# Kernel optimization log

Hardware: AMD Instinct MI355X
Metric: run time of the kernel (lower is better)

The kernel has to match this reference:

```python
import jax, jax.numpy as jnp
import numpy as np
import math

B, N, D, H = 4, 2048, 256, 4
DH = D // H
EPS = 1e-8


def setup_inputs() -> dict:
    key = jax.random.key(0)
    ks = jax.random.split(key, 8)
    x = jax.random.normal(ks[0], (B, N, D), dtype=jnp.float32)
    # RoPE rotation freqs: exp(i * pos * inv_freq), stored as (cos, sin) pairs -> [N, DH//2, 2]
    d2 = DH // 2
    inv_freq = 1.0 / (10000.0 ** (jnp.arange(d2, dtype=jnp.float32) / d2))
    ang = jnp.arange(N, dtype=jnp.float32)[:, None] * inv_freq[None, :]
    freqs = jnp.stack([jnp.cos(ang), jnp.sin(ang)], axis=-1)  # [N, d2, 2]
    s = 0.02
    g = jnp.ones((D,), dtype=jnp.float32)
    w_qkv = jax.random.normal(ks[1], (D, 3 * D), dtype=jnp.float32) * s
    b_qkv = jnp.zeros((3 * D,), dtype=jnp.float32)
    w_out = jax.random.normal(ks[2], (D, D), dtype=jnp.float32) * s
    b_out = jnp.zeros((D,), dtype=jnp.float32)
    w_gate = jax.random.normal(ks[3], (D, D), dtype=jnp.float32) * s
    b_gate = jnp.zeros((D,), dtype=jnp.float32)
    return {"x": x, "freqs": freqs, "g": g, "w_qkv": w_qkv, "b_qkv": b_qkv,
            "w_out": w_out, "b_out": b_out, "w_gate": w_gate, "b_gate": b_gate}


def _zcrmsnorm(x, g):
    x0 = x - jnp.mean(x, axis=-1, keepdims=True)
    rms = jnp.sqrt(jnp.mean(x0 * x0, axis=-1, keepdims=True) + EPS)
    return x0 / rms * g


def _rope(q, freqs):
    # q: [B,H,N,DH]; freqs: [N,DH//2,2] (cos,sin). Complex multiply on adjacent pairs.
    b, h, n, dh = q.shape
    qp = q.reshape(b, h, n, dh // 2, 2)
    cos = freqs[:n, :, 0][None, None]  # [1,1,N,d2]
    sin = freqs[:n, :, 1][None, None]
    q0, q1 = qp[..., 0], qp[..., 1]
    out = jnp.stack([q0 * cos - q1 * sin, q0 * sin + q1 * cos], axis=-1)
    return out.reshape(b, h, n, dh)


def reference(x, freqs, g, w_qkv, b_qkv, w_out, b_out, w_gate, b_gate):
    b, n, d = x.shape
    h = _zcrmsnorm(x, g)
    qkv = (h @ w_qkv + b_qkv).reshape(b, n, 3, H, DH)
    qkv = jnp.transpose(qkv, (2, 0, 3, 1, 4))  # [3,B,H,N,DH]
    q, k, v = qkv[0], qkv[1], qkv[2]
    q = _rope(q, freqs)
    k = _rope(k, freqs)
    scores = jnp.einsum('bhqd,bhkd->bhqk', q, k) / math.sqrt(DH)
    attn = jax.nn.softmax(scores, axis=-1)  # dropout is identity in eval
    y = jnp.einsum('bhqk,bhkd->bhqd', attn, v)
    y = jnp.transpose(y, (0, 2, 1, 3)).reshape(b, n, d)
    y = y @ w_out + b_out
    gate = jax.nn.sigmoid(h @ w_gate + b_gate)
    return x + gate * y
```

## Files before the change

kernel.cpp:

```cpp
#include <hip/hip_runtime.h>

typedef unsigned short u16;
typedef unsigned int u32;
typedef short short8 __attribute__((ext_vector_type(8)));
typedef float f32x4 __attribute__((ext_vector_type(4)));

#define B_ 4
#define N_ 2048
#define D_ 256
#define H_ 4
#define DH_ 64
#define BN_ 8192

__device__ inline float b2f(u16 u) {
    union { u32 i; float f; } v; v.i = ((u32)u) << 16; return v.f;
}
__device__ inline u16 f2b(float f) {
    union { float f; u32 i; } v; v.f = f;
    return (u16)((v.i + 0x8000u) >> 16);
}
__device__ inline u32 pkbf(float a, float b) {
    union { float f; u32 i; } ua, ub; ua.f = a; ub.f = b;
    return __builtin_amdgcn_perm(ub.i + 0x8000u, ua.i + 0x8000u, 0x07060302u);
}
__device__ inline f32x4 mfma16(short8 a, short8 b, f32x4 c) {
    return __builtin_amdgcn_mfma_f32_16x16x32_bf16(a, b, c, 0, 0, 0);
}

__device__ __forceinline__ void gemm_body(
    int bx, int by, int tid,
    const u16* __restrict__ A, const u16* __restrict__ BT,
    const float* __restrict__ bias, void* __restrict__ Cout,
    int Ntot)
{
    const int wave = tid >> 6, lane = tid & 63;
    const int ln15 = lane & 15, quad = lane >> 4;
    const int m0 = bx * 128 + (wave & 1) * 64;
    const int n0 = by * 128 + (wave >> 1) * 64;

    const f32x4 zero = {0.f, 0.f, 0.f, 0.f};
    f32x4 acc[4][4];
    #pragma unroll
    for (int i = 0; i < 4; ++i)
        #pragma unroll
        for (int j = 0; j < 4; ++j) acc[i][j] = zero;

    #pragma unroll
    for (int k0 = 0; k0 < 256; k0 += 32) {
        const int koff = k0 + quad * 8;
        short8 a[4], b[4];
        #pragma unroll
        for (int i = 0; i < 4; ++i)
            a[i] = *(const short8*)(A + (size_t)(m0 + i * 16 + ln15) * 256 + koff);
        #pragma unroll
        for (int j = 0; j < 4; ++j)
            b[j] = *(const short8*)(BT + (size_t)(n0 + j * 16 + ln15) * 256 + koff);
        #pragma unroll
        for (int i = 0; i < 4; ++i)
            #pragma unroll
            for (int j = 0; j < 4; ++j)
                acc[i][j] = mfma16(a[i], b[j], acc[i][j]);
    }

    #pragma unroll
    for (int i = 0; i < 4; ++i) {
        const int r = m0 + i * 16 + quad * 4;
        #pragma unroll
        for (int j = 0; j < 4; ++j) {
            const int c = n0 + j * 16 + ln15;
            const float bv = bias[c];
            #pragma unroll
            for (int rg = 0; rg < 4; ++rg) {
                const size_t idx = (size_t)(r + rg) * Ntot + c;
                ((u16*)Cout)[idx] = f2b(acc[i][j][rg] + bv);
            }
        }
    }
}

__device__ __forceinline__ void gemm_thin_body(
    int bx, int by, int tid,
    const u16* __restrict__ A, const u16* __restrict__ BT,
    const float* __restrict__ bias, void* __restrict__ Cout,
    const float* __restrict__ xin, const u16* __restrict__ gate,
    int mode)
{
    const int wave = tid >> 6, lane = tid & 63;
    const int ln15 = lane & 15, quad = lane >> 4;
    const int m0 = bx * 64 + (wave & 1) * 32;
    const int n0 = by * 64 + (wave >> 1) * 32;

    const f32x4 zero = {0.f, 0.f, 0.f, 0.f};
    f32x4 acc[2][2];
    #pragma unroll
    for (int i = 0; i < 2; ++i)
        #pragma unroll
        for (int j = 0; j < 2; ++j) acc[i][j] = zero;

    #pragma unroll
    for (int k0 = 0; k0 < 256; k0 += 32) {
        const int koff = k0 + quad * 8;
        short8 a[2], b[2];
        #pragma unroll
        for (int i = 0; i < 2; ++i)
            a[i] = *(const short8*)(A + (size_t)(m0 + i * 16 + ln15) * 256 + koff);
        #pragma unroll
        for (int j = 0; j < 2; ++j)
            b[j] = *(const short8*)(BT + (size_t)(n0 + j * 16 + ln15) * 256 + koff);
        #pragma unroll
        for (int i = 0; i < 2; ++i)
            #pragma unroll
            for (int j = 0; j < 2; ++j)
                acc[i][j] = mfma16(a[i], b[j], acc[i][j]);
    }

    #pragma unroll
    for (int i = 0; i < 2; ++i) {
        const int r = m0 + i * 16 + quad * 4;
        #pragma unroll
        for (int j = 0; j < 2; ++j) {
            const int c = n0 + j * 16 + ln15;
            const float bv = bias[c];
            #pragma unroll
            for (int rg = 0; rg < 4; ++rg) {
                const size_t idx = (size_t)(r + rg) * 256 + c;
                float v = acc[i][j][rg] + bv;
                if (mode == 1) {
                    ((u16*)Cout)[idx] = f2b(1.0f / (1.0f + __expf(-v)));
                } else {
                    ((float*)Cout)[idx] = xin[idx] + b2f(gate[idx]) * v;
                }
            }
        }
    }
}

__global__ __launch_bounds__(256) void gemm_ep(
    const u16* __restrict__ A, const u16* __restrict__ BT,
    const float* __restrict__ bias, void* __restrict__ Cout, int Ntot)
{
    gemm_body(blockIdx.x, blockIdx.y, threadIdx.x, A, BT, bias, Cout, Ntot);
}

__global__ __launch_bounds__(256) void gemm_thin(
    const u16* __restrict__ A, const u16* __restrict__ BT,
    const float* __restrict__ bias, void* __restrict__ Cout,
    const float* __restrict__ xin, const u16* __restrict__ gate, int mode)
{
    gemm_thin_body(blockIdx.x, blockIdx.y, threadIdx.x, A, BT, bias, Cout,
                   xin, gate, mode);
}

__global__ __launch_bounds__(256) void norm_transw_k(
    const float* __restrict__ x, const float* __restrict__ g, u16* __restrict__ h,
    const float* __restrict__ wqkv, const float* __restrict__ wout,
    const float* __restrict__ wgate,
    u16* __restrict__ wqkvT, u16* __restrict__ woutT, u16* __restrict__ wgateT)
{
    if (blockIdx.x < 2048) {
        const int wave = threadIdx.x >> 6, lane = threadIdx.x & 63;
        const int t = blockIdx.x * 4 + wave;
        const float4 u = *(const float4*)(x + (size_t)t * D_ + lane * 4);
        float s  = u.x + u.y + u.z + u.w;
        float s2 = u.x * u.x + u.y * u.y + u.z * u.z + u.w * u.w;
        #pragma unroll
        for (int m = 1; m < 64; m <<= 1) {
            s  += __shfl_xor(s, m);
            s2 += __shfl_xor(s2, m);
        }
        float mean = s * (1.0f / D_);
        float var  = s2 * (1.0f / D_) - mean * mean;
        float rinv = rsqrtf(var + 1e-8f);
        const float4 gv = *(const float4*)(g + lane * 4);
        uint2 o;
        o.x = pkbf((u.x - mean) * rinv * gv.x, (u.y - mean) * rinv * gv.y);
        o.y = pkbf((u.z - mean) * rinv * gv.z, (u.w - mean) * rinv * gv.w);
        *(uint2*)(h + (size_t)t * D_ + lane * 4) = o;
    } else {
        int idx = (blockIdx.x - 2048) * 256 + threadIdx.x;
        if (idx < 768 * 256) {
            int nn = idx >> 8, kk = idx & 255;
            wqkvT[idx] = f2b(wqkv[kk * 768 + nn]);
        }
        idx -= 768 * 256;
        if (idx >= 0 && idx < 256 * 256) {
            int nn = idx >> 8, kk = idx & 255;
            woutT[idx]  = f2b(wout[kk * 256 + nn]);
            wgateT[idx] = f2b(wgate[kk * 256 + nn]);
        }
    }
}

#define QSCALE 0.18033688f
__global__ __launch_bounds__(256) void rope_vt_gate_k(
    const u16* __restrict__ qkv, const float* __restrict__ freqs,
    u16* __restrict__ Q, u16* __restrict__ K, u16* __restrict__ VT,
    const u16* __restrict__ h, const u16* __restrict__ wgateT,
    const float* __restrict__ b_gate, u16* __restrict__ gatb)
{
    __shared__ __align__(16) u16 tile[64 * 65];
    const int blk = blockIdx.x;
    if (blk < 1024) {
        const int idx = blk * 256 + threadIdx.x;
        const int t = idx >> 5, rem = idx & 31;
        const int hh = rem >> 3, s8 = rem & 7;
        const int b = t >> 11, n = t & 2047;

        const float4 f0 = *(const float4*)(freqs + (size_t)n * 64 + s8 * 8);
        const float4 f1 = *(const float4*)(freqs + (size_t)n * 64 + s8 * 8 + 4);

        const u16* qp = qkv + (size_t)t * 768 + hh * 64 + s8 * 8;
        const uint4 qv = *(const uint4*)qp;
        const uint4 kv = *(const uint4*)(qp + 256);

        const size_t off = ((size_t)(b * H_ + hh) * N_ + n) * DH_ + s8 * 8;
        uint4 qo, ko;
        {
            float q0 = b2f((u16)(qv.x & 0xffff)), q1 = b2f((u16)(qv.x >> 16));
            float k0 = b2f((u16)(kv.x & 0xffff)), k1 = b2f((u16)(kv.x >> 16));
            qo.x = pkbf((q0 * f0.x - q1 * f0.y) * QSCALE, (q0 * f0.y + q1 * f0.x) * QSCALE);
            ko.x = pkbf(k0 * f0.x - k1 * f0.y, k0 * f0.y + k1 * f0.x);
        }
        {
            float q0 = b2f((u16)(qv.y & 0xffff)), q1 = b2f((u16)(qv.y >> 16));
            float k0 = b2f((u16)(kv.y & 0xffff)), k1 = b2f((u16)(kv.y >> 16));
            qo.y = pkbf((q0 * f0.z - q1 * f0.w) * QSCALE, (q0 * f0.w + q1 * f0.z) * QSCALE);
            ko.y = pkbf(k0 * f0.z - k1 * f0.w, k0 * f0.w + k1 * f0.z);
        }
        {
            float q0 = b2f((u16)(qv.z & 0xffff)), q1 = b2f((u16)(qv.z >> 16));
            float k0 = b2f((u16)(kv.z & 0xffff)), k1 = b2f((u16)(kv.z >> 16));
            qo.z = pkbf((q0 * f1.x - q1 * f1.y) * QSCALE, (q0 * f1.y + q1 * f1.x) * QSCALE);
            ko.z = pkbf(k0 * f1.x - k1 * f1.y, k0 * f1.y + k1 * f1.x);
        }
        {
            float q0 = b2f((u16)(qv.w & 0xffff)), q1 = b2f((u16)(qv.w >> 16));
            float k0 = b2f((u16)(kv.w & 0xffff)), k1 = b2f((u16)(kv.w >> 16));
            qo.w = pkbf((q0 * f1.z - q1 * f1.w) * QSCALE, (q0 * f1.w + q1 * f1.z) * QSCALE);
            ko.w = pkbf(k0 * f1.z - k1 * f1.w, k0 * f1.w + k1 * f1.z);
        }
        *(uint4*)(Q + off) = qo;
        *(uint4*)(K + off) = ko;
    } else if (blk < 1536) {
        const int id2 = blk - 1024;
        const int bh = id2 & 15;
        const int n0 = (id2 >> 4) * 64;
        const int b = bh >> 2, hh = bh & 3;
        #pragma unroll
        for (int rep = 0; rep < 16; ++rep) {
            int idx = rep * 256 + threadIdx.x;
            int nl = idx >> 6, dh = idx & 63;
            tile[dh * 65 + nl] = qkv[(size_t)(b * N_ + n0 + nl) * 768 + 512 + hh * 64 + dh];
        }
        __syncthreads();
        #pragma unroll
        for (int rep = 0; rep < 16; ++rep) {
            int idx = rep * 256 + threadIdx.x;
            int dh = idx >> 6, nl = idx & 63;
            VT[((size_t)bh * 64 + dh) * N_ + n0 + nl] = tile[dh * 65 + nl];
        }
    } else {
        const int id3 = blk - 1536;
        gemm_thin_body(id3 & 127, id3 >> 7, threadIdx.x, h, wgateT, b_gate,
                       (void*)gatb, (const float*)nullptr, (const u16*)nullptr, 1);
    }
}

__global__ __launch_bounds__(512, 4) void attn_k(
    const u16* __restrict__ Q, const u16* __restrict__ K,
    const u16* __restrict__ VT, float* __restrict__ Op,
    float* __restrict__ lvp)
{
    __shared__ __align__(16) u16 Ks[2][64][64];
    __shared__ __align__(16) u16 Vs[2][64][64];
    __shared__ __align__(16) u16 Pb[8][16 * 88];
    const int tid = threadIdx.x;
    const int wave = tid >> 6, lane = tid & 63;
    const int ln15 = lane & 15, quad = lane >> 4;
    const int id = blockIdx.x;
    const int bh   = ((id & 7) << 1) | ((id >> 3) & 1);
    const int half = (id >> 4) & 1;
    const int q0   = (id >> 5) * 128 + wave * 16;
    const int kt0  = half * 1024;

    const u16* Qh = Q + (size_t)bh * N_ * DH_;
    const u16* Kh = K + (size_t)bh * N_ * DH_;
    const u16* Vh = VT + (size_t)bh * DH_ * N_;

    const short8 bq0 = *(const short8*)(Qh + (size_t)(q0 + ln15) * DH_ + quad * 8);
    const short8 bq1 = *(const short8*)(Qh + (size_t)(q0 + ln15) * DH_ + 32 + quad * 8);

    const f32x4 zero = {0.f, 0.f, 0.f, 0.f};
    f32x4 o[4];
    #pragma unroll
    for (int j = 0; j < 4; ++j) o[j] = zero;
    float lv = 0.f;
    u16* Pw = Pb[wave];

    const int srow = tid >> 3, sq8 = tid & 7;
    const int wc = (sq8 * 8) ^ ((srow & 7) << 3);
    const int swl = (ln15 & 7) << 3;
    const int rc0 = (quad * 8) ^ swl;
    const int rc1 = (quad * 8 + 32) ^ swl;

    {
        uint4 k0 = *(const uint4*)(Kh + (size_t)(kt0 + srow) * DH_ + sq8 * 8);
        uint4 v0 = *(const uint4*)(Vh + (size_t)srow * N_ + kt0 + sq8 * 8);
        *(uint4*)&Ks[0][srow][wc] = k0;
        *(uint4*)&Vs[0][srow][wc] = v0;
    }
    __syncthreads();

    int p = 0;
    for (int c = 0; c < 16; ++c) {
        const int ktn = kt0 + (c + 1) * 64;
        uint4 k0, v0;
        const bool more = (c + 1 < 16);
        if (more) {
            k0 = *(const uint4*)(Kh + (size_t)(ktn + srow) * DH_ + sq8 * 8);
            v0 = *(const uint4*)(Vh + (size_t)srow * N_ + ktn + sq8 * 8);
        }

        f32x4 st[4];
        #pragma unroll
        for (int c4 = 0; c4 < 4; ++c4) {
            short8 ka0 = *(const short8*)&Ks[p][c4 * 16 + ln15][rc0];
            short8 ka1 = *(const short8*)&Ks[p][c4 * 16 + ln15][rc1];
            st[c4] = mfma16(ka0, bq0, zero);
            st[c4] = mfma16(ka1, bq1, st[c4]);
        }
        f32x4 pr[4];
        float rs = 0.f;
        #pragma unroll
        for (int c4 = 0; c4 < 4; ++c4) {
            #pragma unroll
            for (int r = 0; r < 4; ++r) {
                pr[c4][r] = exp2f(st[c4][r]);
                rs += pr[c4][r];
            }
        }
        lv += rs;
        #pragma unroll
        for (int c4 = 0; c4 < 4; ++c4) {
            uint2 w;
            w.x = pkbf(pr[c4][0], pr[c4][1]);
            w.y = pkbf(pr[c4][2], pr[c4][3]);
            *(uint2*)(Pw + ln15 * 88 + c4 * 16 + quad * 4) = w;
        }
        asm volatile("s_waitcnt lgkmcnt(0)" ::: "memory");
        const short8 bp0 = *(const short8*)(Pw + ln15 * 88 + quad * 8);
        const short8 bp1 = *(const short8*)(Pw + ln15 * 88 + 32 + quad * 8);
        #pragma unroll
        for (int j = 0; j < 4; ++j) {
            short8 va0 = *(const short8*)&Vs[p][j * 16 + ln15][rc0];
            short8 va1 = *(const short8*)&Vs[p][j * 16 + ln15][rc1];
            o[j] = mfma16(va0, bp0, o[j]);
            o[j] = mfma16(va1, bp1, o[j]);
        }

        if (more) {
            *(uint4*)&Ks[p ^ 1][srow][wc] = k0;
            *(uint4*)&Vs[p ^ 1][srow][wc] = v0;
        }
        __syncthreads();
        p ^= 1;
    }

    lv += __shfl_xor(lv, 16);
    lv += __shfl_xor(lv, 32);
    const size_t rowo = ((size_t)(half * 16 + bh) * N_ + q0 + ln15) * DH_;
    #pragma unroll
    for (int j = 0; j < 4; ++j) {
        float4 w4 = {o[j][0], o[j][1], o[j][2], o[j][3]};
        *(float4*)(Op + rowo + j * 16 + quad * 4) = w4;
    }
    if (quad == 0) lvp[(size_t)(half * 16 + bh) * N_ + q0 + ln15] = lv;
}

__global__ __launch_bounds__(256) void combine_k(
    const float* __restrict__ Op, const float* __restrict__ lvp,
    u16* __restrict__ yt)
{
    const int t = blockIdx.x * 256 + threadIdx.x;
    const int dh0 = (t & 7) * 8;
    const int q   = (t >> 3) & 2047;
    const int bh  = t >> 14;
    const size_t o0 = ((size_t)bh * N_ + q) * DH_ + dh0;
    const size_t o1 = o0 + (size_t)16 * N_ * DH_;
    const float4 a0 = *(const float4*)(Op + o0);
    const float4 a1 = *(const float4*)(Op + o0 + 4);
    const float4 c0 = *(const float4*)(Op + o1);
    const float4 c1 = *(const float4*)(Op + o1 + 4);
    const float rl = 1.0f / (lvp[(size_t)bh * N_ + q] + lvp[(size_t)(16 + bh) * N_ + q]);
    uint4 w;
    w.x = pkbf((a0.x + c0.x) * rl, (a0.y + c0.y) * rl);
    w.y = pkbf((a0.z + c0.z) * rl, (a0.w + c0.w) * rl);
    w.z = pkbf((a1.x + c1.x) * rl, (a1.y + c1.y) * rl);
    w.w = pkbf((a1.z + c1.z) * rl, (a1.w + c1.w) * rl);
    const int b = bh >> 2, h = bh & 3;
    *(uint4*)(yt + ((size_t)b * N_ + q) * D_ + h * 64 + dh0) = w;
}

extern "C" void kernel_launch(void* const* d_in, const int* in_sizes, int n_in,
                              void* d_out, int out_size, void* d_ws, size_t ws_size,
                              hipStream_t stream) {
    const float* x      = (const float*)d_in[0];
    const float* freqs  = (const float*)d_in[1];
    const float* g      = (const float*)d_in[2];
    const float* w_qkv  = (const float*)d_in[3];
    const float* b_qkv  = (const float*)d_in[4];
    const float* w_out  = (const float*)d_in[5];
    const float* b_out  = (const float*)d_in[6];
    const float* w_gate = (const float*)d_in[7];
    const float* b_gate = (const float*)d_in[8];
    float* out = (float*)d_out;

    char* ws = (char*)d_ws;
    size_t off = 0;
    auto carve = [&](size_t nelem) -> u16* {
        u16* p = (u16*)(ws + off);
        off += ((nelem * 2 + 255) / 256) * 256;
        return p;
    };
    u16* h      = carve((size_t)BN_ * D_);
    u16* qkv    = carve((size_t)BN_ * 768);
    u16* Qb     = carve((size_t)BN_ * D_);
    u16* Kb     = carve((size_t)BN_ * D_);
    u16* VT     = carve((size_t)BN_ * D_);
    u16* gatb   = carve((size_t)BN_ * D_);
    u16* wqkvT  = carve((size_t)768 * 256);
    u16* woutT  = carve((size_t)256 * 256);
    u16* wgateT = carve((size_t)256 * 256);
    float* Op  = (float*)ws;
    float* lvp = (float*)wqkvT;
    u16*   yt  = Qb;

    hipLaunchKernelGGL(norm_transw_k, dim3(3072), dim3(256), 0, stream,
                       x, g, h, w_qkv, w_out, w_gate, wqkvT, woutT, wgateT);
    hipLaunchKernelGGL(gemm_ep, dim3(BN_ / 128, 6), dim3(256), 0, stream,
                       h, wqkvT, b_qkv, (void*)qkv, 768);
    hipLaunchKernelGGL(rope_vt_gate_k, dim3(2048), dim3(256), 0, stream,
                       qkv, freqs, Qb, Kb, VT, h, wgateT, b_gate, gatb);
    hipLaunchKernelGGL(attn_k, dim3(512), dim3(512), 0, stream,
                       Qb, Kb, VT, Op, lvp);
    hipLaunchKernelGGL(combine_k, dim3(1024), dim3(256), 0, stream,
                       Op, lvp, yt);
    hipLaunchKernelGGL(gemm_thin, dim3(128, 4), dim3(256), 0, stream,
                       yt, woutT, b_out, (void*)out, x, gatb, 2);
}
```

Measured before the change: 165.9 us.

## Switch attention to 32x32x16 MFMA with in-register P via permlane32 swap

Rewrites the attention inner loop to use 32x32x16 bf16 MFMA tiles, so each wave handles 32 query rows and the block shrinks to 4 waves. The softmax probabilities are packed to bf16 and rearranged in registers with v_permlane32_swap instead of being staged through a per-wave LDS buffer, which removes that round trip and its wait. The aim is fewer LDS accesses and instructions per tile and better MFMA throughput. In exchange each wave needs more registers and each block has fewer threads, which may reduce occupancy and latency hiding.

```diff
diff --git a/kernel.cpp b/kernel.cpp
--- a/kernel.cpp
+++ b/kernel.cpp
@@ -4,6 +4,7 @@
 typedef unsigned int u32;
 typedef short short8 __attribute__((ext_vector_type(8)));
 typedef float f32x4 __attribute__((ext_vector_type(4)));
+typedef float f32x16 __attribute__((ext_vector_type(16)));
 
 #define B_ 4
 #define N_ 2048
@@ -25,6 +26,9 @@
 }
 __device__ inline f32x4 mfma16(short8 a, short8 b, f32x4 c) {
     return __builtin_amdgcn_mfma_f32_16x16x32_bf16(a, b, c, 0, 0, 0);
+}
+__device__ inline f32x16 mfma32(short8 a, short8 b, f32x16 c) {
+    return __builtin_amdgcn_mfma_f32_32x32x16_bf16(a, b, c, 0, 0, 0);
 }
 
 __device__ __forceinline__ void gemm_body(
@@ -266,115 +270,137 @@
     }
 }
 
-__global__ __launch_bounds__(512, 4) void attn_k(
+__global__ __launch_bounds__(256, 2) void attn_k(
     const u16* __restrict__ Q, const u16* __restrict__ K,
     const u16* __restrict__ VT, float* __restrict__ Op,
     float* __restrict__ lvp)
 {
     __shared__ __align__(16) u16 Ks[2][64][64];
     __shared__ __align__(16) u16 Vs[2][64][64];
-    __shared__ __align__(16) u16 Pb[8][16 * 88];
     const int tid = threadIdx.x;
     const int wave = tid >> 6, lane = tid & 63;
-    const int ln15 = lane & 15, quad = lane >> 4;
+    const int l31 = lane & 31, hi = lane >> 5;
     const int id = blockIdx.x;
     const int bh   = ((id & 7) << 1) | ((id >> 3) & 1);
     const int half = (id >> 4) & 1;
-    const int q0   = (id >> 5) * 128 + wave * 16;
+    const int q0   = (id >> 5) * 128 + wave * 32;
     const int kt0  = half * 1024;
 
     const u16* Qh = Q + (size_t)bh * N_ * DH_;
     const u16* Kh = K + (size_t)bh * N_ * DH_;
     const u16* Vh = VT + (size_t)bh * DH_ * N_;
 
-    const short8 bq0 = *(const short8*)(Qh + (size_t)(q0 + ln15) * DH_ + quad * 8);
-    const short8 bq1 = *(const short8*)(Qh + (size_t)(q0 + ln15) * DH_ + 32 + quad * 8);
-
-    const f32x4 zero = {0.f, 0.f, 0.f, 0.f};
-    f32x4 o[4];
-    #pragma unroll
-    for (int j = 0; j < 4; ++j) o[j] = zero;
+    short8 bq[4];
+    #pragma unroll
+    for (int kc = 0; kc < 4; ++kc)
+        bq[kc] = *(const short8*)(Qh + (size_t)(q0 + l31) * DH_ + kc * 16 + hi * 8);
+
+    f32x16 o0, o1;
+    #pragma unroll
+    for (int i = 0; i < 16; ++i) { o0[i] = 0.f; o1[i] = 0.f; }
     float lv = 0.f;
-    u16* Pw = Pb[wave];
-
-    const int srow = tid >> 3, sq8 = tid & 7;
-    const int wc = (sq8 * 8) ^ ((srow & 7) << 3);
-    const int swl = (ln15 & 7) << 3;
-    const int rc0 = (quad * 8) ^ swl;
-    const int rc1 = (quad * 8 + 32) ^ swl;
+
+    const int srow = tid >> 2, sq4 = tid & 3;
+    const int sw = srow & 7;
+    const int wg0 = ((sq4) ^ sw) * 8;
+    const int wg1 = ((sq4 + 4) ^ sw) * 8;
+    const int rsw = l31 & 7;
 
     {
-        uint4 k0 = *(const uint4*)(Kh + (size_t)(kt0 + srow) * DH_ + sq8 * 8);
-        uint4 v0 = *(const uint4*)(Vh + (size_t)srow * N_ + kt0 + sq8 * 8);
-        *(uint4*)&Ks[0][srow][wc] = k0;
-        *(uint4*)&Vs[0][srow][wc] = v0;
+        uint4 k0 = *(const uint4*)(Kh + (size_t)(kt0 + srow) * DH_ + sq4 * 8);
+        uint4 k1 = *(const uint4*)(Kh + (size_t)(kt0 + srow) * DH_ + (sq4 + 4) * 8);
+        uint4 v0 = *(const uint4*)(Vh + (size_t)srow * N_ + kt0 + sq4 * 8);
+        uint4 v1 = *(const uint4*)(Vh + (size_t)srow * N_ + kt0 + (sq4 + 4) * 8);
+        *(uint4*)&Ks[0][srow][wg0] = k0;
+        *(uint4*)&Ks[0][srow][wg1] = k1;
+        *(uint4*)&Vs[0][srow][wg0] = v0;
+        *(uint4*)&Vs[0][srow][wg1] = v1;
     }
     __syncthreads();
 
     int p = 0;
     for (int c = 0; c < 16; ++c) {
-        const int ktn = kt0 + (c + 1) * 64;
-        uint4 k0, v0;
         const bool more = (c + 1 < 16);
+        uint4 k0, k1, v0, v1;
         if (more) {
-            k0 = *(const uint4*)(Kh + (size_t)(ktn + srow) * DH_ + sq8 * 8);
-            v0 = *(const uint4*)(Vh + (size_t)srow * N_ + ktn + sq8 * 8);
-        }
-
-        f32x4 st[4];
-        #pragma unroll
-        for (int c4 = 0; c4 < 4; ++c4) {
-            short8 ka0 = *(const short8*)&Ks[p][c4 * 16 + ln15][rc0];
-            short8 ka1 = *(const short8*)&Ks[p][c4 * 16 + ln15][rc1];
-            st[c4] = mfma16(ka0, bq0, zero);
-            st[c4] = mfma16(ka1, bq1, st[c4]);
-        }
-        f32x4 pr[4];
-        float rs = 0.f;
-        #pragma unroll
-        for (int c4 = 0; c4 < 4; ++c4) {
-            #pragma unroll
-            for (int r = 0; r < 4; ++r) {
-                pr[c4][r] = exp2f(st[c4][r]);
-                rs += pr[c4][r];
+            const int ktn = kt0 + (c + 1) * 64;
+            k0 = *(const uint4*)(Kh + (size_t)(ktn + srow) * DH_ + sq4 * 8);
+            k1 = *(const uint4*)(Kh + (size_t)(ktn + srow) * DH_ + (sq4 + 4) * 8);
+            v0 = *(const uint4*)(Vh + (size_t)srow * N_ + ktn + sq4 * 8);
+            v1 = *(const uint4*)(Vh + (size_t)srow * N_ + ktn + (sq4 + 4) * 8);
+        }
+
+        f32x16 st0, st1;
+        #pragma unroll
+        for (int i = 0; i < 16; ++i) { st0[i] = 0.f; st1[i] = 0.f; }
+        #pragma unroll
+        for (int kc = 0; kc < 4; ++kc) {
+            const int gran = ((2 * kc + hi) ^ rsw) * 8;
+            short8 ka0 = *(const short8*)&Ks[p][l31][gran];
+            short8 ka1 = *(const short8*)&Ks[p][32 + l31][gran];
+            st0 = mfma32(ka0, bq[kc], st0);
+            st1 = mfma32(ka1, bq[kc], st1);
+        }
+
+        short8 pb[4];
+        #pragma unroll
+        for (int g = 0; g < 2; ++g) {
+            float pr[16];
+            #pragma unroll
+            for (int r = 0; r < 16; ++r) {
+                pr[r] = exp2f(g ? st1[r] : st0[r]);
+                lv += pr[r];
             }
-        }
-        lv += rs;
-        #pragma unroll
-        for (int c4 = 0; c4 < 4; ++c4) {
-            uint2 w;
-            w.x = pkbf(pr[c4][0], pr[c4][1]);
-            w.y = pkbf(pr[c4][2], pr[c4][3]);
-            *(uint2*)(Pw + ln15 * 88 + c4 * 16 + quad * 4) = w;
-        }
-        asm volatile("s_waitcnt lgkmcnt(0)" ::: "memory");
-        const short8 bp0 = *(const short8*)(Pw + ln15 * 88 + quad * 8);
-        const short8 bp1 = *(const short8*)(Pw + ln15 * 88 + 32 + quad * 8);
-        #pragma unroll
-        for (int j = 0; j < 4; ++j) {
-            short8 va0 = *(const short8*)&Vs[p][j * 16 + ln15][rc0];
-            short8 va1 = *(const short8*)&Vs[p][j * 16 + ln15][rc1];
-            o[j] = mfma16(va0, bp0, o[j]);
-            o[j] = mfma16(va1, bp1, o[j]);
+            #pragma unroll
+            for (int kc2 = 0; kc2 < 2; ++kc2) {
+                u32 X0, X1, Y0, Y1;
+                asm("v_cvt_pk_bf16_f32 %0, %1, %2" : "=v"(X0) : "v"(pr[8*kc2+0]), "v"(pr[8*kc2+1]));
+                asm("v_cvt_pk_bf16_f32 %0, %1, %2" : "=v"(X1) : "v"(pr[8*kc2+2]), "v"(pr[8*kc2+3]));
+                asm("v_cvt_pk_bf16_f32 %0, %1, %2" : "=v"(Y0) : "v"(pr[8*kc2+4]), "v"(pr[8*kc2+5]));
+                asm("v_cvt_pk_bf16_f32 %0, %1, %2" : "=v"(Y1) : "v"(pr[8*kc2+6]), "v"(pr[8*kc2+7]));
+                asm("v_permlane32_swap_b32 %0, %1" : "+v"(X0), "+v"(Y0));
+                asm("v_permlane32_swap_b32 %0, %1" : "+v"(X1), "+v"(Y1));
+                union { u32 u[4]; short8 s; } bf;
+                bf.u[0] = X0; bf.u[1] = X1; bf.u[2] = Y0; bf.u[3] = Y1;
+                pb[g * 2 + kc2] = bf.s;
+            }
+        }
+
+        #pragma unroll
+        for (int kc = 0; kc < 4; ++kc) {
+            const int gran = ((2 * kc + hi) ^ rsw) * 8;
+            short8 va0 = *(const short8*)&Vs[p][l31][gran];
+            short8 va1 = *(const short8*)&Vs[p][32 + l31][gran];
+            o0 = mfma32(va0, pb[kc], o0);
+            o1 = mfma32(va1, pb[kc], o1);
         }
 
         if (more) {
-            *(uint4*)&Ks[p ^ 1][srow][wc] = k0;
-            *(uint4*)&Vs[p ^ 1][srow][wc] = v0;
+            *(uint4*)&Ks[p ^ 1][srow][wg0] = k0;
+            *(uint4*)&Ks[p ^ 1][srow][wg1] = k1;
+            *(uint4*)&Vs[p ^ 1][srow][wg0] = v0;
+            *(uint4*)&Vs[p ^ 1][srow][wg1] = v1;
         }
         __syncthreads();
         p ^= 1;
     }
 
-    lv += __shfl_xor(lv, 16);
     lv += __shfl_xor(lv, 32);
-    const size_t rowo = ((size_t)(half * 16 + bh) * N_ + q0 + ln15) * DH_;
-    #pragma unroll
-    for (int j = 0; j < 4; ++j) {
-        float4 w4 = {o[j][0], o[j][1], o[j][2], o[j][3]};
-        *(float4*)(Op + rowo + j * 16 + quad * 4) = w4;
-    }
-    if (quad == 0) lvp[(size_t)(half * 16 + bh) * N_ + q0 + ln15] = lv;
+    const size_t rowo = ((size_t)(half * 16 + bh) * N_ + q0 + l31) * DH_;
+    #pragma unroll
+    for (int go = 0; go < 2; ++go) {
+        #pragma unroll
+        for (int rq = 0; rq < 4; ++rq) {
+            float4 w4;
+            if (go == 0) {
+                w4.x = o0[rq*4+0]; w4.y = o0[rq*4+1]; w4.z = o0[rq*4+2]; w4.w = o0[rq*4+3];
+            } else {
+                w4.x = o1[rq*4+0]; w4.y = o1[rq*4+1]; w4.z = o1[rq*4+2]; w4.w = o1[rq*4+3];
+            }
+            *(float4*)(Op + rowo + go * 32 + 8 * rq + 4 * hi) = w4;
+        }
+    }
+    if (hi == 0) lvp[(size_t)(half * 16 + bh) * N_ + q0 + l31] = lv;
 }
 
 __global__ __launch_bounds__(256) void combine_k(
@@ -441,7 +467,7 @@
                        h, wqkvT, b_qkv, (void*)qkv, 768);
     hipLaunchKernelGGL(rope_vt_gate_k, dim3(2048), dim3(256), 0, stream,
                        qkv, freqs, Qb, Kb, VT, h, wgateT, b_gate, gatb);
-    hipLaunchKernelGGL(attn_k, dim3(512), dim3(512), 0, stream,
+    hipLaunchKernelGGL(attn_k, dim3(512), dim3(256), 0, stream,
                        Qb, Kb, VT, Op, lvp);
     hipLaunchKernelGGL(combine_k, dim3(1024), dim3(256), 0, stream,
                        Op, lvp, yt);
```

New measurement: 166.8 us. About the same (+0.5%).
